# Kernel tuning notes

Hardware: AMD Instinct MI355X
Metric: run time of the kernel (lower is better)

The kernel has to match this reference:

```python
import jax, jax.numpy as jnp
import numpy as np

N_HEAD = 16
HEAD_SIZE = 64

def setup_inputs() -> dict:
    key = jax.random.key(0)
    ks = jax.random.split(key, 5)
    B, T, C = 2, 2048, 1024
    s = 0.02
    return {
        "x": jax.random.normal(ks[0], (B, T, C), dtype=jnp.float32),
        "We": jax.random.normal(ks[1], (3 * C, C), dtype=jnp.float32) * s,
        "be": jax.random.normal(ks[2], (3 * C,), dtype=jnp.float32) * s,
        "Wp": jax.random.normal(ks[3], (C, C), dtype=jnp.float32) * s,
        "bp": jax.random.normal(ks[4], (C,), dtype=jnp.float32) * s,
    }

def reference(x, We, be, Wp, bp):
    B, T, C = x.shape
    H, D = N_HEAD, HEAD_SIZE
    qkv = x @ We.T + be                      # [B,T,3C]
    q, k, v = jnp.split(qkv, 3, axis=-1)
    # [B,H,T,D]
    q = q.reshape(B, T, H, D).transpose(0, 2, 1, 3)
    k = k.reshape(B, T, H, D).transpose(0, 2, 1, 3)
    v = v.reshape(B, T, H, D).transpose(0, 2, 1, 3)
    scale = 1.0 / jnp.sqrt(jnp.asarray(D, dtype=x.dtype))
    att = jnp.einsum('bhqd,bhkd->bhqk', q, k) * scale
    causal = jnp.tril(jnp.ones((T, T), dtype=bool))
    att = jnp.where(causal, att, -jnp.inf)
    att = jax.nn.softmax(att, axis=-1)
    y = jnp.einsum('bhqk,bhkd->bhqd', att, v)   # [B,H,T,D]
    y = y.transpose(0, 2, 1, 3).reshape(B, T, C)
    return y @ Wp.T + bp
```

## Files before the change

kernel.cpp:

```cpp
#include <hip/hip_runtime.h>
#include <hip/hip_bf16.h>
#include <stdint.h>
#include <stddef.h>

typedef short s8v __attribute__((ext_vector_type(8)));
typedef float f4v __attribute__((ext_vector_type(4)));

__device__ inline float b2f(short s) {
    union { unsigned u; float f; } x;
    x.u = ((unsigned)(unsigned short)s) << 16;
    return x.f;
}
__device__ inline short f2b(float f) {
    union { float f; unsigned u; } x;
    x.f = f;
    unsigned r = x.u + 0x7FFF + ((x.u >> 16) & 1);
    return (short)(r >> 16);
}

__device__ __forceinline__ void gl16(const short* g, short* l) {
    __builtin_amdgcn_global_load_lds(
        (const __attribute__((address_space(1))) void*)g,
        (__attribute__((address_space(3))) void*)l,
        16, 0, 0);
}

__global__ void detect_dtype(const unsigned* __restrict__ x, int* __restrict__ flag)
{
    int hit = 0;
    for (int i = threadIdx.x; i < 1024; i += 64) {
        unsigned lo = x[i] & 0xFFFFu;
        unsigned e = (lo >> 7) & 0xFFu;
        if (e >= 0x8Au) hit = 1;
    }
    unsigned long long any = __ballot(hit != 0);
    if (threadIdx.x == 0) *flag = (any != 0ull) ? 1 : 0;
}

__global__ __launch_bounds__(256) void convert_bf16(
    const void* s0, short* d0, size_t c0,
    const void* s1, short* d1, size_t c1,
    const void* s2, short* d2, size_t c2,
    const void* s3, short* d3, size_t c3,
    const void* s4, short* d4, size_t c4,
    const int* __restrict__ flagp)
{
    const bool f32 = (*flagp != 0);
    const void* srcs[5] = {s0, s1, s2, s3, s4};
    short* dsts[5] = {d0, d1, d2, d3, d4};
    size_t cnts[5] = {c0, c1, c2, c3, c4};
    size_t total = c0 + c1 + c2 + c3 + c4;
    size_t stride = (size_t)gridDim.x * blockDim.x;
    for (size_t c = (size_t)blockIdx.x * blockDim.x + threadIdx.x; c < total; c += stride) {
        size_t r = c; int s = 0;
        while (r >= cnts[s]) { r -= cnts[s]; s++; }
        short* d = dsts[s] + r * 8;
        if (f32) {
            const float* p = (const float*)srcs[s] + r * 8;
            f4v a = *(const f4v*)p;
            f4v b = *(const f4v*)(p + 4);
            s8v v;
            v[0] = f2b(a[0]); v[1] = f2b(a[1]); v[2] = f2b(a[2]); v[3] = f2b(a[3]);
            v[4] = f2b(b[0]); v[5] = f2b(b[1]); v[6] = f2b(b[2]); v[7] = f2b(b[3]);
            *(s8v*)d = v;
        } else {
            *(s8v*)d = *(const s8v*)((const short*)srcs[s] + r * 8);
        }
    }
}

#define BM 128
#define BKK 64

template<int QKV, int TBN>
__global__ __launch_bounds__(256) void gemm_bt_bias(
    const short* __restrict__ A,
    const short* __restrict__ B,
    const short* __restrict__ bias,
    void* __restrict__ C,
    short* __restrict__ vT,
    int M, int N, int K, int ldc,
    const int* __restrict__ flagp, int oDyn)
{
    const bool of32 = oDyn && (*flagp != 0);
    const int NT = TBN / 32;

    __shared__ __align__(16) short smem[QKV ? (128 * 136) : (BM + TBN) * BKK];
    short* sA = smem;
    short* sB = smem + BM * BKK;

    const int tid  = threadIdx.x;
    const int lane = tid & 63;
    const int w    = tid >> 6;
    const int wm   = (w >> 1) * 64;
    const int wn   = (w & 1) * (TBN / 2);
    const int quad = lane >> 4;
    const int l16  = lane & 15;

    const int m0 = blockIdx.y * BM;
    const int n0 = blockIdx.x * TBN;

    f4v acc[4][NT];
    const f4v vzero = {0.0f, 0.0f, 0.0f, 0.0f};
#pragma unroll
    for (int i = 0; i < 4; i++)
#pragma unroll
        for (int j = 0; j < NT; j++) acc[i][j] = vzero;

    for (int k0 = 0; k0 < K; k0 += BKK) {
        __syncthreads();
#pragma unroll
        for (int i = 0; i < 4; i++) {
            int c  = i * 256 + tid;
            int r  = c >> 3, kk = (c & 7) * 8;
            int cb = i * 256 + (tid & 192);
            gl16(A + (size_t)(m0 + r) * K + k0 + kk, sA + cb * 8);
            if (i < TBN / 32)
                gl16(B + (size_t)(n0 + r) * K + k0 + kk, sB + cb * 8);
        }
        __syncthreads();
#pragma unroll
        for (int s = 0; s < 2; s++) {
            s8v af[4], bf[NT];
#pragma unroll
            for (int t = 0; t < 4; t++)
                af[t] = *(const s8v*)(sA + (wm + t * 16 + l16) * BKK + s * 32 + quad * 8);
#pragma unroll
            for (int t = 0; t < NT; t++)
                bf[t] = *(const s8v*)(sB + (wn + t * 16 + l16) * BKK + s * 32 + quad * 8);
#pragma unroll
            for (int mt = 0; mt < 4; mt++)
#pragma unroll
                for (int nt = 0; nt < NT; nt++)
                    acc[mt][nt] = __builtin_amdgcn_mfma_f32_16x16x32_bf16(
                        af[mt], bf[nt], acc[mt][nt], 0, 0, 0);
        }
    }

    if (QKV && n0 >= 2048) {
        __syncthreads();
#pragma unroll
        for (int nt = 0; nt < NT; nt++) {
            int nl = wn + nt * 16 + l16;
            float bv = b2f(bias[n0 + nl]);
#pragma unroll
            for (int mt = 0; mt < 4; mt++)
#pragma unroll
                for (int r = 0; r < 4; r++) {
                    int ml = wm + mt * 16 + quad * 4 + r;
                    smem[nl * 136 + ml] = f2b(acc[mt][nt][r] + bv);
                }
        }
        __syncthreads();
        int nl = tid >> 1, half = tid & 1;
        int n = n0 + nl;
        int h = (n - 2048) >> 6, d = n & 63;
        int bq = m0 >> 11;
        short* dst = vT + (((size_t)(bq * 16 + h)) * 64 + d) * 2048 + (m0 & 2047) + half * 64;
        const short* src = smem + nl * 136 + half * 64;
#pragma unroll
        for (int j = 0; j < 8; j++)
            *(s8v*)(dst + j * 8) = *(const s8v*)(src + j * 8);
    } else {
        const float osc = (QKV && n0 < 1024) ? 0.125f : 1.0f;
#pragma unroll
        for (int nt = 0; nt < NT; nt++) {
            int n = n0 + wn + nt * 16 + l16;
            float bv = b2f(bias[n]);
#pragma unroll
            for (int mt = 0; mt < 4; mt++) {
#pragma unroll
                for (int r = 0; r < 4; r++) {
                    int m = m0 + wm + mt * 16 + quad * 4 + r;
                    float v = (acc[mt][nt][r] + bv) * osc;
                    if (of32) ((float*)C)[(size_t)m * ldc + n] = v;
                    else      ((short*)C)[(size_t)m * ldc + n] = f2b(v);
                }
            }
        }
    }
}

#define LP 72

template<int PARTS>
__global__ __launch_bounds__(256) void attn_flash(
    const short* __restrict__ qk,
    const short* __restrict__ vt,
    short* __restrict__ y,
    short* __restrict__ Opart,
    float* __restrict__ Lpart)
{
    const int T = 2048, LDQ = 2048;
    __shared__ __align__(16) short sK[64 * LP];
    __shared__ __align__(16) short sVT[64 * LP];
    __shared__ __align__(16) short sP[4][16 * LP];

    const int tid  = threadIdx.x;
    const int lane = tid & 63;
    const int w    = tid >> 6;
    const int quad = lane >> 4;
    const int l16  = lane & 15;

    int part, qt, bh, u;
    if (PARTS == 2) {
        part = blockIdx.x & 1;
        int rest = blockIdx.x >> 1;
        qt = 31 - (rest >> 5);
        bh = rest & 31;
        u  = bh * 32 + qt;
    } else {
        part = 0;
        qt = 31 - (blockIdx.x >> 5);
        bh = blockIdx.x & 31;
        u  = 0;
    }
    const int b = bh >> 4;
    const int h = bh & 15;

    const int n    = qt + 1;
    const int half = (n + 1) >> 1;
    const int klo  = (PARTS == 2 && part) ? half : 0;
    const int khi  = (PARTS == 2 && !part) ? half : n;

    if (PARTS == 2 && klo >= khi) {
        s8v z;
#pragma unroll
        for (int j = 0; j < 8; j++) z[j] = 0;
        s8v* ob = (s8v*)(Opart + ((size_t)(part * 1024 + u)) * 4096);
        for (int i = tid; i < 512; i += 256) ob[i] = z;
        if (tid < 64) Lpart[(size_t)(part * 1024 + u) * 64 + tid] = 0.0f;
        return;
    }

    const size_t qkbase = (size_t)b * T * LDQ;
    const short* Kbase  = qk + qkbase + 1024 + h * 64;
    const short* Vbase  = vt + (size_t)bh * 64 * 2048;

    s8v qf[2];
    {
        int qrow = qt * 64 + w * 16 + l16;
        const short* qp = qk + qkbase + (size_t)qrow * LDQ + h * 64 + quad * 8;
        qf[0] = *(const s8v*)(qp);
        qf[1] = *(const s8v*)(qp + 32);
    }

    const f4v vzero = {0.0f, 0.0f, 0.0f, 0.0f};
    f4v o[4];
#pragma unroll
    for (int i = 0; i < 4; i++) o[i] = vzero;
    float lsum[4] = {0.0f, 0.0f, 0.0f, 0.0f};

    for (int kt = klo; kt < khi; kt++) {
        __syncthreads();
#pragma unroll
        for (int i = 0; i < 2; i++) {
            int c = i * 256 + tid;
            int r = c >> 3, dd = (c & 7) * 8;
            s8v kv = *(const s8v*)(Kbase + (size_t)(kt * 64 + r) * LDQ + dd);
            s8v vv = *(const s8v*)(Vbase + (size_t)r * 2048 + kt * 64 + dd);
            *(s8v*)(sK  + r * LP + dd) = kv;
            *(s8v*)(sVT + r * LP + dd) = vv;
        }
        __syncthreads();

        f4v sacc[4];
#pragma unroll
        for (int nt = 0; nt < 4; nt++) {
            sacc[nt] = vzero;
            s8v kf0 = *(const s8v*)(sK + (nt * 16 + l16) * LP + quad * 8);
            s8v kf1 = *(const s8v*)(sK + (nt * 16 + l16) * LP + 32 + quad * 8);
            sacc[nt] = __builtin_amdgcn_mfma_f32_16x16x32_bf16(qf[0], kf0, sacc[nt], 0, 0, 0);
            sacc[nt] = __builtin_amdgcn_mfma_f32_16x16x32_bf16(qf[1], kf1, sacc[nt], 0, 0, 0);
        }

        short* pp = sP[w];
        const bool diag = (kt == qt);
#pragma unroll
        for (int nt = 0; nt < 4; nt++) {
#pragma unroll
            for (int r = 0; r < 4; r++) {
                float p = __expf(sacc[nt][r]);
                if (diag) {
                    int q = w * 16 + quad * 4 + r;
                    int k = nt * 16 + l16;
                    if (k > q) p = 0.0f;
                }
                union { float f; unsigned u; } c; c.f = p;
                short p16 = (short)(c.u >> 16);
                c.u &= 0xFFFF0000u;
                lsum[r] += c.f;
                pp[(quad * 4 + r) * LP + nt * 16 + l16] = p16;
            }
        }
        __syncthreads();

        s8v pf0 = *(const s8v*)(pp + l16 * LP + quad * 8);
        s8v pf1 = *(const s8v*)(pp + l16 * LP + 32 + quad * 8);
#pragma unroll
        for (int dt = 0; dt < 4; dt++) {
            s8v vf0 = *(const s8v*)(sVT + (dt * 16 + l16) * LP + quad * 8);
            s8v vf1 = *(const s8v*)(sVT + (dt * 16 + l16) * LP + 32 + quad * 8);
            o[dt] = __builtin_amdgcn_mfma_f32_16x16x32_bf16(pf0, vf0, o[dt], 0, 0, 0);
            o[dt] = __builtin_amdgcn_mfma_f32_16x16x32_bf16(pf1, vf1, o[dt], 0, 0, 0);
        }
    }

#pragma unroll
    for (int r = 0; r < 4; r++) {
        float s = lsum[r];
        s += __shfl_xor(s, 1, 64);
        s += __shfl_xor(s, 2, 64);
        s += __shfl_xor(s, 4, 64);
        s += __shfl_xor(s, 8, 64);
        lsum[r] = s;
    }

    if (PARTS == 2) {
        short* ob = Opart + ((size_t)(part * 1024 + u)) * 4096;
#pragma unroll
        for (int dt = 0; dt < 4; dt++)
#pragma unroll
            for (int r = 0; r < 4; r++)
                ob[(w * 16 + quad * 4 + r) * 64 + dt * 16 + l16] = f2b(o[dt][r]);
        if (l16 == 0) {
#pragma unroll
            for (int r = 0; r < 4; r++)
                Lpart[(size_t)(part * 1024 + u) * 64 + w * 16 + quad * 4 + r] = lsum[r];
        }
    } else {
#pragma unroll
        for (int r = 0; r < 4; r++) lsum[r] = 1.0f / lsum[r];
#pragma unroll
        for (int dt = 0; dt < 4; dt++)
#pragma unroll
            for (int r = 0; r < 4; r++) {
                int qrow = qt * 64 + w * 16 + quad * 4 + r;
                int d = dt * 16 + l16;
                y[((size_t)b * T + qrow) * 1024 + h * 64 + d] = f2b(o[dt][r] * lsum[r]);
            }
    }
}

__global__ __launch_bounds__(256) void attn_combine(
    const short* __restrict__ Opart,
    const float* __restrict__ Lpart,
    short* __restrict__ y)
{
    const int u  = blockIdx.x;
    const int bh = u >> 5, qt = u & 31;
    const int b = bh >> 4, h = bh & 15;
    const int t = threadIdx.x;
    const int q = t >> 2, dg = (t & 3) * 16;

    float l = Lpart[(size_t)u * 64 + q] + Lpart[(size_t)(1024 + u) * 64 + q];
    float rl = 1.0f / l;
    const short* p0 = Opart + (size_t)u * 4096 + q * 64 + dg;
    const short* p1 = Opart + (size_t)(1024 + u) * 4096 + q * 64 + dg;
    short* yo = y + ((size_t)b * 2048 + qt * 64 + q) * 1024 + h * 64 + dg;
#pragma unroll
    for (int hv = 0; hv < 2; hv++) {
        s8v a = *(const s8v*)(p0 + hv * 8);
        s8v c = *(const s8v*)(p1 + hv * 8);
        s8v r;
#pragma unroll
        for (int j = 0; j < 8; j++) r[j] = f2b((b2f(a[j]) + b2f(c[j])) * rl);
        *(s8v*)(yo + hv * 8) = r;
    }
}

extern "C" void kernel_launch(void* const* d_in, const int* in_sizes, int n_in,
                              void* d_out, int out_size, void* d_ws, size_t ws_size,
                              hipStream_t stream)
{
    char* p = (char*)d_ws;
    int*   flag = (int*)p;                 p += 16;
    short* qk   = (short*)p;               p += (size_t)4096 * 2048 * 2;
    short* vT   = (short*)p;               p += (size_t)32 * 64 * 2048 * 2;
    short* xb   = (short*)p;               p += (size_t)4096 * 1024 * 2;
    short* Web  = (short*)p;               p += (size_t)3072 * 1024 * 2;
    short* Wpb  = (short*)p;               p += (size_t)1024 * 1024 * 2;
    short* beb  = (short*)p;               p += 3072 * 2;
    short* bpb  = (short*)p;               p += 1024 * 2;
    short* Opart = (short*)p;              p += (size_t)2 * 1024 * 4096 * 2;
    float* Lpart = (float*)p;              p += (size_t)2 * 1024 * 64 * 4;
    short* y = xb;
    const size_t need = (size_t)(p - (char*)d_ws);
    const bool split = (ws_size >= need);

    detect_dtype<<<1, 64, 0, stream>>>((const unsigned*)d_in[0], flag);

    convert_bf16<<<dim3(4098), 256, 0, stream>>>(
        d_in[0], xb,  (size_t)4096 * 1024 / 8,
        d_in[1], Web, (size_t)3072 * 1024 / 8,
        d_in[2], beb, (size_t)3072 / 8,
        d_in[3], Wpb, (size_t)1024 * 1024 / 8,
        d_in[4], bpb, (size_t)1024 / 8,
        flag);

    gemm_bt_bias<1, 128><<<dim3(3072 / 128, 4096 / BM), 256, 0, stream>>>(
        xb, Web, beb, qk, vT, 4096, 3072, 1024, 2048, flag, 0);

    if (split) {
        attn_flash<2><<<dim3(2048), 256, 0, stream>>>(qk, vT, nullptr, Opart, Lpart);
        attn_combine<<<dim3(1024), 256, 0, stream>>>(Opart, Lpart, y);
    } else {
        attn_flash<1><<<dim3(1024), 256, 0, stream>>>(qk, vT, y, nullptr, nullptr);
    }

    gemm_bt_bias<0, 64><<<dim3(1024 / 64, 4096 / BM), 256, 0, stream>>>(
        y, Wpb, bpb, d_out, nullptr, 4096, 1024, 1024, 1024, flag, 1);
}
```

Baseline: 216.5 us.

## Shrink GEMM M-tile to 64 and fold dtype detection into convert kernel

Parameterizes the GEMM on tile M size and occupancy hint, switching both projection GEMMs from 128-row to 64-row tiles so the grid has twice as many blocks on the many-CU device. The V-transpose epilogue is adapted to the smaller tile with a 72-stride LDS staging buffer. The separate dtype-detection launch is removed; each convert block now samples the input itself and block 0 writes the flag for later kernels. Smaller tiles reduce per-block reuse of loaded operands and add redundant detection reads in every convert block.

Result: faster. 205.5 us (-5.1%).

```diff
diff --git a/kernel.cpp b/kernel.cpp
--- a/kernel.cpp
+++ b/kernel.cpp
@@ -23,18 +23,6 @@
         (const __attribute__((address_space(1))) void*)g,
         (__attribute__((address_space(3))) void*)l,
         16, 0, 0);
-}
-
-__global__ void detect_dtype(const unsigned* __restrict__ x, int* __restrict__ flag)
-{
-    int hit = 0;
-    for (int i = threadIdx.x; i < 1024; i += 64) {
-        unsigned lo = x[i] & 0xFFFFu;
-        unsigned e = (lo >> 7) & 0xFFu;
-        if (e >= 0x8Au) hit = 1;
-    }
-    unsigned long long any = __ballot(hit != 0);
-    if (threadIdx.x == 0) *flag = (any != 0ull) ? 1 : 0;
 }
 
 __global__ __launch_bounds__(256) void convert_bf16(
@@ -43,9 +31,17 @@
     const void* s2, short* d2, size_t c2,
     const void* s3, short* d3, size_t c3,
     const void* s4, short* d4, size_t c4,
-    const int* __restrict__ flagp)
+    int* __restrict__ flagout)
 {
-    const bool f32 = (*flagp != 0);
+    int hit = 0;
+    const unsigned* xw = (const unsigned*)s0;
+    for (int i = threadIdx.x & 63; i < 1024; i += 64) {
+        unsigned e = ((xw[i] & 0xFFFFu) >> 7) & 0xFFu;
+        if (e >= 0x8Au) hit = 1;
+    }
+    const bool f32 = (__ballot(hit != 0) != 0ull);
+    if (blockIdx.x == 0 && threadIdx.x == 0) *flagout = f32 ? 1 : 0;
+
     const void* srcs[5] = {s0, s1, s2, s3, s4};
     short* dsts[5] = {d0, d1, d2, d3, d4};
     size_t cnts[5] = {c0, c1, c2, c3, c4};
@@ -69,11 +65,10 @@
     }
 }
 
-#define BM 128
 #define BKK 64
 
-template<int QKV, int TBN>
-__global__ __launch_bounds__(256) void gemm_bt_bias(
+template<int QKV, int TBM, int TBN, int MINW>
+__global__ __launch_bounds__(256, MINW) void gemm_bt_bias(
     const short* __restrict__ A,
     const short* __restrict__ B,
     const short* __restrict__ bias,
@@ -83,53 +78,58 @@
     const int* __restrict__ flagp, int oDyn)
 {
     const bool of32 = oDyn && (*flagp != 0);
-    const int NT = TBN / 32;
-
-    __shared__ __align__(16) short smem[QKV ? (128 * 136) : (BM + TBN) * BKK];
+    const int MT = TBM / 32, NT = TBN / 32;
+
+    __shared__ __align__(16) short smem[(TBM + TBN) * BKK];
     short* sA = smem;
-    short* sB = smem + BM * BKK;
+    short* sB = smem + TBM * BKK;
 
     const int tid  = threadIdx.x;
     const int lane = tid & 63;
     const int w    = tid >> 6;
-    const int wm   = (w >> 1) * 64;
+    const int wm   = (w >> 1) * (TBM / 2);
     const int wn   = (w & 1) * (TBN / 2);
     const int quad = lane >> 4;
     const int l16  = lane & 15;
 
-    const int m0 = blockIdx.y * BM;
+    const int m0 = blockIdx.y * TBM;
     const int n0 = blockIdx.x * TBN;
 
-    f4v acc[4][NT];
+    f4v acc[MT][NT];
     const f4v vzero = {0.0f, 0.0f, 0.0f, 0.0f};
 #pragma unroll
-    for (int i = 0; i < 4; i++)
+    for (int i = 0; i < MT; i++)
 #pragma unroll
         for (int j = 0; j < NT; j++) acc[i][j] = vzero;
 
+    const int ACH = TBM * 8;
     for (int k0 = 0; k0 < K; k0 += BKK) {
         __syncthreads();
 #pragma unroll
-        for (int i = 0; i < 4; i++) {
+        for (int i = 0; i < (TBM + TBN) / 32; i++) {
             int c  = i * 256 + tid;
-            int r  = c >> 3, kk = (c & 7) * 8;
             int cb = i * 256 + (tid & 192);
-            gl16(A + (size_t)(m0 + r) * K + k0 + kk, sA + cb * 8);
-            if (i < TBN / 32)
-                gl16(B + (size_t)(n0 + r) * K + k0 + kk, sB + cb * 8);
+            if (c < ACH) {
+                int r = c >> 3, kk = (c & 7) * 8;
+                gl16(A + (size_t)(m0 + r) * K + k0 + kk, sA + cb * 8);
+            } else {
+                int c2 = c - ACH, cb2 = cb - ACH;
+                int r = c2 >> 3, kk = (c2 & 7) * 8;
+                gl16(B + (size_t)(n0 + r) * K + k0 + kk, sB + cb2 * 8);
+            }
         }
         __syncthreads();
 #pragma unroll
         for (int s = 0; s < 2; s++) {
-            s8v af[4], bf[NT];
-#pragma unroll
-            for (int t = 0; t < 4; t++)
+            s8v af[MT], bf[NT];
+#pragma unroll
+            for (int t = 0; t < MT; t++)
                 af[t] = *(const s8v*)(sA + (wm + t * 16 + l16) * BKK + s * 32 + quad * 8);
 #pragma unroll
             for (int t = 0; t < NT; t++)
                 bf[t] = *(const s8v*)(sB + (wn + t * 16 + l16) * BKK + s * 32 + quad * 8);
 #pragma unroll
-            for (int mt = 0; mt < 4; mt++)
+            for (int mt = 0; mt < MT; mt++)
 #pragma unroll
                 for (int nt = 0; nt < NT; nt++)
                     acc[mt][nt] = __builtin_amdgcn_mfma_f32_16x16x32_bf16(
@@ -138,17 +138,18 @@
     }
 
     if (QKV && n0 >= 2048) {
+        static_assert(!QKV || TBM == 64, "V transpose assumes TBM==64");
         __syncthreads();
 #pragma unroll
         for (int nt = 0; nt < NT; nt++) {
             int nl = wn + nt * 16 + l16;
             float bv = b2f(bias[n0 + nl]);
 #pragma unroll
-            for (int mt = 0; mt < 4; mt++)
+            for (int mt = 0; mt < MT; mt++)
 #pragma unroll
                 for (int r = 0; r < 4; r++) {
                     int ml = wm + mt * 16 + quad * 4 + r;
-                    smem[nl * 136 + ml] = f2b(acc[mt][nt][r] + bv);
+                    smem[nl * 72 + ml] = f2b(acc[mt][nt][r] + bv);
                 }
         }
         __syncthreads();
@@ -156,10 +157,10 @@
         int n = n0 + nl;
         int h = (n - 2048) >> 6, d = n & 63;
         int bq = m0 >> 11;
-        short* dst = vT + (((size_t)(bq * 16 + h)) * 64 + d) * 2048 + (m0 & 2047) + half * 64;
-        const short* src = smem + nl * 136 + half * 64;
-#pragma unroll
-        for (int j = 0; j < 8; j++)
+        short* dst = vT + (((size_t)(bq * 16 + h)) * 64 + d) * 2048 + (m0 & 2047) + half * 32;
+        const short* src = smem + nl * 72 + half * 32;
+#pragma unroll
+        for (int j = 0; j < 4; j++)
             *(s8v*)(dst + j * 8) = *(const s8v*)(src + j * 8);
     } else {
         const float osc = (QKV && n0 < 1024) ? 0.125f : 1.0f;
@@ -168,7 +169,7 @@
             int n = n0 + wn + nt * 16 + l16;
             float bv = b2f(bias[n]);
 #pragma unroll
-            for (int mt = 0; mt < 4; mt++) {
+            for (int mt = 0; mt < MT; mt++) {
 #pragma unroll
                 for (int r = 0; r < 4; r++) {
                     int m = m0 + wm + mt * 16 + quad * 4 + r;
@@ -388,8 +389,6 @@
     const size_t need = (size_t)(p - (char*)d_ws);
     const bool split = (ws_size >= need);
 
-    detect_dtype<<<1, 64, 0, stream>>>((const unsigned*)d_in[0], flag);
-
     convert_bf16<<<dim3(4098), 256, 0, stream>>>(
         d_in[0], xb,  (size_t)4096 * 1024 / 8,
         d_in[1], Web, (size_t)3072 * 1024 / 8,
@@ -398,7 +397,7 @@
         d_in[4], bpb, (size_t)1024 / 8,
         flag);
 
-    gemm_bt_bias<1, 128><<<dim3(3072 / 128, 4096 / BM), 256, 0, stream>>>(
+    gemm_bt_bias<1, 64, 128, 6><<<dim3(3072 / 128, 4096 / 64), 256, 0, stream>>>(
         xb, Web, beb, qk, vT, 4096, 3072, 1024, 2048, flag, 0);
 
     if (split) {
@@ -408,6 +407,6 @@
         attn_flash<1><<<dim3(1024), 256, 0, stream>>>(qk, vT, y, nullptr, nullptr);
     }
 
-    gemm_bt_bias<0, 64><<<dim3(1024 / 64, 4096 / BM), 256, 0, stream>>>(
+    gemm_bt_bias<0, 64, 64, 4><<<dim3(1024 / 64, 4096 / 64), 256, 0, stream>>>(
         y, Wpb, bpb, d_out, nullptr, 4096, 1024, 1024, 1024, flag, 1);
 }
```
